# Performance work log

Measured on AMD Instinct MI355X. Metric: run time of the kernel, lower is better.

Reference implementation:

```python
import jax, jax.numpy as jnp
import numpy as np

B, N = 64, 256          # batch, numatoms
ATOMEMB = 20            # hardcoded atomemb_dim
DFEAT = 25              # gaussian centers: arange(0.0, 5.0, 0.2)
MU_MIN, MU_MAX, DELTA_MU, SIGMA = 0.0, 5.0, 0.2, 0.5


def setup_inputs() -> dict:
    key = jax.random.key(0)
    ks = jax.random.split(key, 8)
    s = 0.1
    z = jax.random.randint(ks[0], (B, N), 0, N)
    dist = jax.random.uniform(ks[1], (B, N, N), dtype=jnp.float32) * 5.0
    emb = jax.random.normal(ks[2], (N, ATOMEMB), dtype=jnp.float32) * s
    Vw = jax.random.normal(ks[3], (ATOMEMB, ATOMEMB + DFEAT), dtype=jnp.float32) * s
    Vb = jnp.zeros((ATOMEMB,), dtype=jnp.float32)
    W1 = jax.random.normal(ks[4], (10, ATOMEMB), dtype=jnp.float32) * s
    b1 = jnp.zeros((10,), dtype=jnp.float32)
    W2 = jax.random.normal(ks[5], (1, 10), dtype=jnp.float32) * s
    b2 = jnp.zeros((1,), dtype=jnp.float32)
    return dict(z=z, dist=dist, emb=emb, Vw=Vw, Vb=Vb, W1=W1, b1=b1, W2=W2, b2=b2)


def reference(z, dist, emb, Vw, Vb, W1, b1, W2, b2):
    mask = (z != 0).astype(dist.dtype)                      # [B,N]
    cfeat = emb[z] * mask[..., None]                        # [B,N,20]
    # expand atom features over neighbor axis j and re-apply i-mask (as in source)
    cexp = jnp.broadcast_to(cfeat[:, :, None, :], (B, N, N, ATOMEMB))
    cexp = cexp * mask[:, :, None, None]
    # Gaussian RBF expansion of pairwise distances -> [B,N,N,25]
    mus = jnp.arange(MU_MIN, MU_MAX, DELTA_MU, dtype=dist.dtype)
    dfeat = jnp.exp(-((dist[..., None] - mus) ** 2) / (2.0 * SIGMA ** 2))
    pair = jnp.concatenate([cexp, dfeat], axis=-1)          # [B,N,N,45]
    # message MLP V: Linear(45->20) + Tanh, masked on atom i
    msg = jnp.tanh(jnp.einsum('bijf,of->bijo', pair, Vw) + Vb)
    msg = msg * mask[:, :, None, None]
    agg = msg.sum(axis=2)                                   # sum over neighbors j
    c = cfeat + agg                                         # [B,N,20]
    # top: Tanh -> Linear(20->10) -> Linear(10->1)
    h = jnp.tanh(c) @ W1.T + b1
    e = h @ W2.T + b2                                       # [B,N,1]
    return e.sum(axis=1).squeeze(-1)                        # [B]
```

## Files before the change

kernel.cpp:

```cpp
#include <hip/hip_runtime.h>

#define Bsz 64
#define Nn  256
#define Ee  20
#define Dd  25
#define NBLK 2048

using short8  = __attribute__((ext_vector_type(8))) short;
using floatx4 = __attribute__((ext_vector_type(4))) float;

#if __has_builtin(__builtin_amdgcn_exp2f)
#define EXP2F(x) __builtin_amdgcn_exp2f(x)
#else
#define EXP2F(x) __expf(0.6931471805599453f * (x))
#endif
#if __has_builtin(__builtin_amdgcn_rcpf)
#define RCPF(x) __builtin_amdgcn_rcpf(x)
#else
#define RCPF(x) (1.0f / (x))
#endif

__device__ __forceinline__ short f2bf(float x) {
    unsigned u = __float_as_uint(x);
    unsigned r = (u + 0x7FFFu + ((u >> 16) & 1u)) >> 16;
    return (short)r;
}
__device__ __forceinline__ float bf2f(short h) {
    return __uint_as_float(((unsigned)(unsigned short)h) << 16);
}
__device__ __forceinline__ float tanhfast(float x) {
    float e = __expf(2.0f * x);
    return 1.0f - 2.0f / (e + 1.0f);
}
__device__ __forceinline__ unsigned packbf(float a, float b) {
#if __has_builtin(__builtin_amdgcn_perm)
    return __builtin_amdgcn_perm(__float_as_uint(b) + 0x8000u,
                                 __float_as_uint(a) + 0x8000u, 0x07060302u);
#else
    unsigned ua = (__float_as_uint(a) + 0x8000u) >> 16;
    unsigned ub = (__float_as_uint(b) + 0x8000u) & 0xFFFF0000u;
    return ua | ub;
#endif
}

__global__ __launch_bounds__(256, 4) void dtnn_main(
    const int*   __restrict__ z,
    const float* __restrict__ dist,
    const float* __restrict__ emb,
    const float* __restrict__ Vw,
    const float* __restrict__ Vb,
    const float* __restrict__ W1,
    const float* __restrict__ W2,
    float*       __restrict__ part)
{
    const int tid  = threadIdx.x;
    const int lane = tid & 63;
    const int wave = tid >> 6;
    const int blk  = blockIdx.x;
    const int b    = blk >> 5;
    const int i0   = ((blk & 31) << 3) | (wave << 1);

    const int c16  = lane & 15;
    const int quad = lane >> 4;
    const int k0   = quad * 8;
    const float Kc = 2.8853900817779268f;
    const float T04 = 1.1541560327111707f;

    const float* dpl = dist + ((size_t)b * Nn + i0) * Nn + c16;

    const int zi0 = z[b * Nn + i0];
    const int zi1 = z[b * Nn + i0 + 1];
    const int zu0 = __builtin_amdgcn_readfirstlane(zi0);
    const int zu1 = __builtin_amdgcn_readfirstlane(zi1);
    const float m0 = (zu0 != 0) ? 1.0f : 0.0f;
    const float m1 = (zu1 != 0) ? 1.0f : 0.0f;

    const float cj[8] = {1.0f, 0.9231163463866358f, 0.7261490370736909f,
                         0.48675225595997157f, 0.2780373004531941f,
                         0.1353352832366127f, 0.05613476283303940f,
                         0.019841459768337877f};

    short8 whiK[2], wloK[2];
    floatx4 bias0[2], bias1[2];
    #pragma unroll
    for (int nt = 0; nt < 2; ++nt) {
        const int o = nt * 16 + c16;
        const bool valid = (o < Ee);
        const int oc = valid ? o : 0;
        #pragma unroll
        for (int jj = 0; jj < 8; ++jj) {
            const int k = k0 + jj;
            const float v = (valid && k < Dd)
                          ? Kc * cj[jj] * Vw[oc * 45 + 20 + k] : 0.0f;
            const short h = f2bf(v);
            whiK[nt][jj] = h;
            wloK[nt][jj] = f2bf(v - bf2f(h));
        }
        float dot0 = 0.0f, dot1 = 0.0f;
        #pragma unroll
        for (int f = 0; f < Ee; ++f) {
            const float w = valid ? Vw[oc * 45 + f] : 0.0f;
            dot0 = fmaf(w, emb[zu0 * Ee + f], dot0);
            dot1 = fmaf(w, emb[zu1 * Ee + f], dot1);
        }
        const float vb = valid ? Vb[oc] : 0.0f;
        const float A0 = Kc * (vb + m0 * dot0);
        const float A1 = Kc * (vb + m1 * dot1);
        bias0[nt] = (floatx4){A0, A0, A0, A0};
        bias1[nt] = (floatx4){A1, A1, A1, A1};
    }

    const float mu0 = 0.2f * (float)k0;
    float Rm0 = 0.0f, Rm1 = 0.0f;
    float Rt0 = 0.0f, Rt1 = 0.0f;

    float d0 = dpl[0];
    float d1 = dpl[Nn];

    #pragma unroll 2
    for (int t = 0; t < 16; ++t) {
        const float d0c = d0, d1c = d1;
        const int tn = (t + 1) & 15;
        d0 = dpl[16 * tn];
        d1 = dpl[Nn + 16 * tn];

        short8 gA, gB;
        {
            const float u = d0c - mu0;
            const float g0 = EXP2F((-Kc * u) * u);
            const float tp = EXP2F(T04 * u);
            const float t2 = tp * tp, t3 = t2 * tp, t4 = t2 * t2;
            const float x1 = g0 * tp, x2 = g0 * t2, x3 = g0 * t3, x4 = g0 * t4;
            union { short8 s; unsigned u4[4]; } G;
            G.u4[0] = packbf(g0, x1);
            G.u4[1] = packbf(x2, x3);
            G.u4[2] = packbf(x4, x1 * t4);
            G.u4[3] = packbf(x2 * t4, x3 * t4);
            gA = G.s;
        }
        {
            const float u = d1c - mu0;
            const float g0 = EXP2F((-Kc * u) * u);
            const float tp = EXP2F(T04 * u);
            const float t2 = tp * tp, t3 = t2 * tp, t4 = t2 * t2;
            const float x1 = g0 * tp, x2 = g0 * t2, x3 = g0 * t3, x4 = g0 * t4;
            union { short8 s; unsigned u4[4]; } G;
            G.u4[0] = packbf(g0, x1);
            G.u4[1] = packbf(x2, x3);
            G.u4[2] = packbf(x4, x1 * t4);
            G.u4[3] = packbf(x2 * t4, x3 * t4);
            gB = G.s;
        }

        floatx4 p00 = __builtin_amdgcn_mfma_f32_16x16x32_bf16(gA, whiK[0], bias0[0], 0, 0, 0);
        p00 = __builtin_amdgcn_mfma_f32_16x16x32_bf16(gA, wloK[0], p00, 0, 0, 0);
        floatx4 p01 = __builtin_amdgcn_mfma_f32_16x16x32_bf16(gA, whiK[1], bias0[1], 0, 0, 0);
        p01 = __builtin_amdgcn_mfma_f32_16x16x32_bf16(gA, wloK[1], p01, 0, 0, 0);
        floatx4 p10 = __builtin_amdgcn_mfma_f32_16x16x32_bf16(gB, whiK[0], bias1[0], 0, 0, 0);
        p10 = __builtin_amdgcn_mfma_f32_16x16x32_bf16(gB, wloK[0], p10, 0, 0, 0);
        floatx4 p11 = __builtin_amdgcn_mfma_f32_16x16x32_bf16(gB, whiK[1], bias1[1], 0, 0, 0);
        p11 = __builtin_amdgcn_mfma_f32_16x16x32_bf16(gB, wloK[1], p11, 0, 0, 0);

        int r0 = __float_as_int(p01[0]);
        r0 = __builtin_amdgcn_update_dpp(r0, __float_as_int(p01[1]), 0x114, 0xF, 0x2, false);
        r0 = __builtin_amdgcn_update_dpp(r0, __float_as_int(p01[2]), 0x118, 0xF, 0x4, false);
        r0 = __builtin_amdgcn_update_dpp(r0, __float_as_int(p01[3]), 0x11C, 0xF, 0x8, false);
        const float At0 = EXP2F(__int_as_float(r0)) + 1.0f;

        int r1 = __float_as_int(p11[0]);
        r1 = __builtin_amdgcn_update_dpp(r1, __float_as_int(p11[1]), 0x114, 0xF, 0x2, false);
        r1 = __builtin_amdgcn_update_dpp(r1, __float_as_int(p11[2]), 0x118, 0xF, 0x4, false);
        r1 = __builtin_amdgcn_update_dpp(r1, __float_as_int(p11[3]), 0x11C, 0xF, 0x8, false);
        const float At1 = EXP2F(__int_as_float(r1)) + 1.0f;

        {
            const float A0 = EXP2F(p00[0]) + 1.0f, A1 = EXP2F(p00[1]) + 1.0f;
            const float A2 = EXP2F(p00[2]) + 1.0f, A3 = EXP2F(p00[3]) + 1.0f;
            const float q01 = A0 * A1, q23 = A2 * A3;
            const float n4  = fmaf(q01, A2 + A3, q23 * (A0 + A1));
            const float d4  = q01 * q23;
            const float inv = RCPF(d4 * At0);
            Rm0 = fmaf(n4 * At0, inv, Rm0);
            Rt0 = fmaf(d4, inv, Rt0);
        }
        {
            const float A0 = EXP2F(p10[0]) + 1.0f, A1 = EXP2F(p10[1]) + 1.0f;
            const float A2 = EXP2F(p10[2]) + 1.0f, A3 = EXP2F(p10[3]) + 1.0f;
            const float q01 = A0 * A1, q23 = A2 * A3;
            const float n4  = fmaf(q01, A2 + A3, q23 * (A0 + A1));
            const float d4  = q01 * q23;
            const float inv = RCPF(d4 * At1);
            Rm1 = fmaf(n4 * At1, inv, Rm1);
            Rt1 = fmaf(d4, inv, Rt1);
        }
    }

    Rm0 += __shfl_xor(Rm0, 16, 64);  Rm0 += __shfl_xor(Rm0, 32, 64);
    Rm1 += __shfl_xor(Rm1, 16, 64);  Rm1 += __shfl_xor(Rm1, 32, 64);
    Rt0 += __shfl_xor(Rt0, 4, 64);   Rt0 += __shfl_xor(Rt0, 8, 64);
    Rt0 += __shfl_xor(Rt0, 16, 64);  Rt0 += __shfl_xor(Rt0, 32, 64);
    Rt1 += __shfl_xor(Rt1, 4, 64);   Rt1 += __shfl_xor(Rt1, 8, 64);
    Rt1 += __shfl_xor(Rt1, 16, 64);  Rt1 += __shfl_xor(Rt1, 32, 64);

    const int om = c16;
    const int ot = 16 + (lane & 3);
    float uom = 0.0f, uot = 0.0f;
    #pragma unroll
    for (int p = 0; p < 10; ++p) {
        uom = fmaf(W2[p], W1[p * Ee + om], uom);
        uot = fmaf(W2[p], W1[p * Ee + ot], uot);
    }
    const float cfm0 = m0 * emb[zu0 * Ee + om];
    const float cfm1 = m1 * emb[zu1 * Ee + om];
    const float cft0 = m0 * emb[zu0 * Ee + ot];
    const float cft1 = m1 * emb[zu1 * Ee + ot];

    float e = 0.0f;
    e = fmaf(tanhfast(cfm0 + m0 * (256.0f - 2.0f * Rm0)), uom, e);
    e = fmaf(tanhfast(cfm1 + m1 * (256.0f - 2.0f * Rm1)), uom, e);
    e = fmaf(tanhfast(cft0 + m0 * (256.0f - 2.0f * Rt0)), 0.25f * uot, e);
    e = fmaf(tanhfast(cft1 + m1 * (256.0f - 2.0f * Rt1)), 0.25f * uot, e);
    e += __shfl_xor(e, 1, 64);
    e += __shfl_xor(e, 2, 64);
    e += __shfl_xor(e, 4, 64);
    e += __shfl_xor(e, 8, 64);

    __shared__ float sE[4];
    if (lane == 0) sE[wave] = e;
    __syncthreads();
    if (tid == 0)
        part[blk] = sE[0] + sE[1] + sE[2] + sE[3];
}

__global__ __launch_bounds__(64) void dtnn_reduce(
    const float* __restrict__ part,
    const float* __restrict__ b1, const float* __restrict__ W2,
    const float* __restrict__ b2, float* __restrict__ out)
{
    const int b = blockIdx.x;
    const int t = threadIdx.x;
    float v = (t < 32) ? part[b * 32 + t] : 0.0f;
    v += __shfl_xor(v, 1, 64);
    v += __shfl_xor(v, 2, 64);
    v += __shfl_xor(v, 4, 64);
    v += __shfl_xor(v, 8, 64);
    v += __shfl_xor(v, 16, 64);
    if (t == 0) {
        float c0 = b2[0];
        #pragma unroll
        for (int p = 0; p < 10; ++p) c0 = fmaf(W2[p], b1[p], c0);
        out[b] = v + __shfl(v, 32, 64) * 0.0f + 256.0f * c0 + __shfl_xor(v, 32, 64);
    }
}

extern "C" void kernel_launch(void* const* d_in, const int* in_sizes, int n_in,
                              void* d_out, int out_size, void* d_ws, size_t ws_size,
                              hipStream_t stream) {
    const int*   z    = (const int*)  d_in[0];
    const float* dist = (const float*)d_in[1];
    const float* emb  = (const float*)d_in[2];
    const float* Vw   = (const float*)d_in[3];
    const float* Vb   = (const float*)d_in[4];
    const float* W1   = (const float*)d_in[5];
    const float* b1   = (const float*)d_in[6];
    const float* W2   = (const float*)d_in[7];
    const float* b2   = (const float*)d_in[8];
    float* out = (float*)d_out;

    float* partP = (float*)d_ws;

    dtnn_main<<<NBLK, 256, 0, stream>>>(z, dist, emb, Vw, Vb, W1, W2, partP);
    dtnn_reduce<<<Bsz, 64, 0, stream>>>(partP, b1, W2, b2, out);
}
```

Measured before the change: 120.2 us.

## Stage distance rows in LDS and pack bf16 with hardware convert

At kernel start each wave issues coalesced loads of its two full distance rows, then stores them into per-wave shared memory. The main loop reads its distances from LDS instead of doing strided prefetch loads from global memory, and the loop is fully unrolled. The float-to-bf16 packing now uses the v_cvt_pk_bf16_f32 instruction via inline asm instead of add-and-permute. The loop reads LDS without a barrier, which relies on each wave reading only its own slice, and the inline asm needs an ISA that supports the instruction.

```diff
diff --git a/kernel.cpp b/kernel.cpp
--- a/kernel.cpp
+++ b/kernel.cpp
@@ -33,14 +33,9 @@
     return 1.0f - 2.0f / (e + 1.0f);
 }
 __device__ __forceinline__ unsigned packbf(float a, float b) {
-#if __has_builtin(__builtin_amdgcn_perm)
-    return __builtin_amdgcn_perm(__float_as_uint(b) + 0x8000u,
-                                 __float_as_uint(a) + 0x8000u, 0x07060302u);
-#else
-    unsigned ua = (__float_as_uint(a) + 0x8000u) >> 16;
-    unsigned ub = (__float_as_uint(b) + 0x8000u) & 0xFFFF0000u;
-    return ua | ub;
-#endif
+    unsigned r;
+    asm("v_cvt_pk_bf16_f32 %0, %1, %2" : "=v"(r) : "v"(a), "v"(b));
+    return r;
 }
 
 __global__ __launch_bounds__(256, 4) void dtnn_main(
@@ -66,7 +61,14 @@
     const float Kc = 2.8853900817779268f;
     const float T04 = 1.1541560327111707f;
 
-    const float* dpl = dist + ((size_t)b * Nn + i0) * Nn + c16;
+    __shared__ float sD[4][2][256];
+    float* sDw = &sD[wave][0][0];
+
+    const float* dr0 = dist + ((size_t)b * Nn + i0) * Nn;
+    const float a0r = dr0[lane],        a1r = dr0[lane + 64];
+    const float a2r = dr0[lane + 128],  a3r = dr0[lane + 192];
+    const float b0r = dr0[Nn + lane],       b1r = dr0[Nn + lane + 64];
+    const float b2r = dr0[Nn + lane + 128], b3r = dr0[Nn + lane + 192];
 
     const int zi0 = z[b * Nn + i0];
     const int zi1 = z[b * Nn + i0 + 1];
@@ -110,19 +112,19 @@
         bias1[nt] = (floatx4){A1, A1, A1, A1};
     }
 
+    sDw[lane]       = a0r;  sDw[lane + 64]  = a1r;
+    sDw[lane + 128] = a2r;  sDw[lane + 192] = a3r;
+    sDw[256 + lane]       = b0r;  sDw[256 + lane + 64]  = b1r;
+    sDw[256 + lane + 128] = b2r;  sDw[256 + lane + 192] = b3r;
+
     const float mu0 = 0.2f * (float)k0;
     float Rm0 = 0.0f, Rm1 = 0.0f;
     float Rt0 = 0.0f, Rt1 = 0.0f;
 
-    float d0 = dpl[0];
-    float d1 = dpl[Nn];
-
-    #pragma unroll 2
+    #pragma unroll
     for (int t = 0; t < 16; ++t) {
-        const float d0c = d0, d1c = d1;
-        const int tn = (t + 1) & 15;
-        d0 = dpl[16 * tn];
-        d1 = dpl[Nn + 16 * tn];
+        const float d0c = sDw[16 * t + c16];
+        const float d1c = sDw[256 + 16 * t + c16];
 
         short8 gA, gB;
         {
```

Result: faster. 114.2 us (-5.0%).
